# Kernel tuning notes

Measured on AMD Instinct MI355X. Metric: run time of the kernel, lower is better.

## Reference

```python
import math
import jax, jax.numpy as jnp
from jax import lax
import numpy as np

D = 256; H = 8; NL = 6; HALF = D // 2
B = 32; NEV = 256

def sinpos(x):
    # SinusoidalPosEmb: (..., ) int -> (..., D)
    freq = jnp.exp(jnp.arange(HALF, dtype=jnp.float32) * (-math.log(10000.0) / (HALF - 1)))
    e = x.astype(jnp.float32)[..., None] * freq
    return jnp.concatenate([jnp.sin(e), jnp.cos(e)], axis=-1)

def layer_norm(x, g, b, eps=1e-5):
    m = x.mean(-1, keepdims=True)
    v = ((x - m) ** 2).mean(-1, keepdims=True)
    return (x - m) / jnp.sqrt(v + eps) * g + b

def gelu(x):
    return jax.nn.gelu(x, approximate=False)

def conv1d(x, w, b, stride):
    y = lax.conv_general_dilated(x, w, (stride,), [(3, 3)], dimension_numbers=("NCH", "OIH", "NCH"))
    return y + b[None, :, None]

def setup_inputs():
    ks = iter(jax.random.split(jax.random.key(0), 48))
    def p(*shape):
        return jax.random.normal(next(ks), shape, dtype=jnp.float32) * 0.02
    inp = dict(
        mel=jax.random.normal(next(ks), (B, 80, 2000), dtype=jnp.float32),
        events=jnp.sort(jax.random.randint(next(ks), (B, NEV), 0, 2000), axis=-1),
        event_mask=jnp.zeros((B, NEV), dtype=bool),
        star_rating=jax.random.uniform(next(ks), (B,), dtype=jnp.float32) * 9.0,
        mel_W=p(16, 80), mel_b=p(16),
        conv1_w=p(128, 16, 7), conv1_b=p(128),
        gn_g=jnp.ones(128, jnp.float32), gn_b=jnp.zeros(128, jnp.float32),
        conv2_w=p(256, 128, 7), conv2_b=p(256),
        cn_g=jnp.ones(D, jnp.float32), cn_b=jnp.zeros(D, jnp.float32),
        star_table=p(20, D),
        ep_W1=p(D, 3 * D), ep_b1=p(D), ep_W2=p(D, D), ep_b2=p(D),
        tl_Wqkv=p(NL, 3 * D, D), tl_bqkv=p(NL, 3 * D),
        tl_Wo=p(NL, D, D), tl_bo=p(NL, D),
        tl_ln1g=jnp.ones((NL, D), jnp.float32), tl_ln1b=jnp.zeros((NL, D), jnp.float32),
        tl_ln2g=jnp.ones((NL, D), jnp.float32), tl_ln2b=jnp.zeros((NL, D), jnp.float32),
        tl_W1=p(NL, 4 * D, D), tl_b1=p(NL, 4 * D),
        tl_W2=p(NL, D, 4 * D), tl_b2=p(NL, D),
        pool_q=jax.random.normal(next(ks), (D,), dtype=jnp.float32),
        on_g=jnp.ones(D, jnp.float32), on_b=jnp.zeros(D, jnp.float32),
        oh_W=p(1, D), oh_b=p(1),
    )
    return inp

def reference(mel, events, event_mask, star_rating, mel_W, mel_b, conv1_w, conv1_b, gn_g, gn_b, conv2_w, conv2_b, cn_g, cn_b, star_table, ep_W1, ep_b1, ep_W2, ep_b2, tl_Wqkv, tl_bqkv, tl_Wo, tl_bo, tl_ln1g, tl_ln1b, tl_ln2g, tl_ln2b, tl_W1, tl_b1, tl_W2, tl_b2, pool_q, on_g, on_b, oh_W, oh_b):
    Bsz = mel.shape[0]
    # mel_compress on channel dim: (B,80,T) -> (B,16,T)
    x_mel = jnp.einsum('bct,oc->bot', mel, mel_W) + mel_b[None, :, None]
    h = gelu(conv1d(x_mel, conv1_w, conv1_b, 2))           # (B,128,1000)
    # GroupNorm(1, C): normalize over (C, L) per sample
    m = h.mean((1, 2), keepdims=True)
    v = ((h - m) ** 2).mean((1, 2), keepdims=True)
    h = (h - m) / jnp.sqrt(v + 1e-5) * gn_g[None, :, None] + gn_b[None, :, None]
    h = gelu(conv1d(h, conv2_w, conv2_b, 2))               # (B,256,500)
    x = h.transpose(0, 2, 1)                               # (B,500,256)
    x = layer_norm(x, cn_g, cn_b)
    S = x.shape[1]
    x = x + sinpos(jnp.arange(S))[None]
    star_bucket = jnp.clip((star_rating / 0.5).astype(jnp.int32), 0, star_table.shape[0] - 1)
    x = x + star_table[star_bucket][:, None, :]
    # --- event gap/ratio embeddings (vectorized; exact match to torch loop when all valid) ---
    diff = jnp.maximum(events[:, 1:] - events[:, :-1], 1)  # clamp(min=1)
    g = jnp.concatenate([diff[:, :1], diff], axis=1)        # g[0] = g[1]
    gap_ms = g * 5
    g_f = jnp.maximum(g.astype(jnp.float32), 1.0)
    r = jnp.clip(g_f[:, 1:] / g_f[:, :-1], 0.1, 10.0)
    ones = jnp.ones((Bsz, 1), dtype=jnp.float32)
    ratio_before = (jnp.concatenate([ones, r], axis=1) * 50).astype(jnp.int32)
    ratio_after = (jnp.concatenate([r, ones], axis=1) * 50).astype(jnp.int32)
    combined = jnp.concatenate([sinpos(ratio_before), sinpos(ratio_after), sinpos(gap_ms)], axis=-1)
    ev = gelu(combined @ ep_W1.T + ep_b1) @ ep_W2.T + ep_b2
    ev = jnp.where(event_mask[..., None], 0.0, ev)
    token_pos = jnp.clip(events // 4, 0, S - 1)
    # batched scatter-add of event embeddings into token stream
    x = x.at[jnp.arange(Bsz)[:, None], token_pos].add(ev)
    hd = D // H
    for i in range(NL):
        xn = layer_norm(x, tl_ln1g[i], tl_ln1b[i])
        qkv = xn @ tl_Wqkv[i].T + tl_bqkv[i]
        q, k, vv = jnp.split(qkv, 3, axis=-1)
        q = q.reshape(Bsz, S, H, hd).transpose(0, 2, 1, 3)
        k = k.reshape(Bsz, S, H, hd).transpose(0, 2, 1, 3)
        vv = vv.reshape(Bsz, S, H, hd).transpose(0, 2, 1, 3)
        a = jax.nn.softmax(jnp.einsum('bhqd,bhkd->bhqk', q, k) / math.sqrt(hd), axis=-1)
        o = jnp.einsum('bhqk,bhkd->bhqd', a, vv).transpose(0, 2, 1, 3).reshape(Bsz, S, D)
        x = x + o @ tl_Wo[i].T + tl_bo[i]
        xn = layer_norm(x, tl_ln2g[i], tl_ln2b[i])
        x = x + gelu(xn @ tl_W1[i].T + tl_b1[i]) @ tl_W2[i].T + tl_b2[i]
    # attention pooling + head
    logits = x @ pool_q / math.sqrt(D)
    w = jax.nn.softmax(logits, axis=-1)
    pooled = jnp.einsum('bs,bsd->bd', w, x)
    return (layer_norm(pooled, on_g, on_b) @ oh_W.T + oh_b).squeeze(-1)
```

## Files before the change

### kernel.cpp

```cpp
#include <hip/hip_runtime.h>
#include <math.h>

namespace {
constexpr int kB = 32;
constexpr int kS = 500;
constexpr int kH = 8;
}
#define LKC (-0.07252236513366287)

typedef __attribute__((ext_vector_type(8))) short s16x8;
typedef __attribute__((ext_vector_type(4))) float f32x4;

__device__ __forceinline__ float gelu_f(float x){
  return 0.5f * x * (1.0f + erff(x * 0.7071067811865476f));
}
__device__ __forceinline__ float b2f(short s){
  union { unsigned u; float f; } x; x.u = ((unsigned)(unsigned short)s) << 16; return x.f;
}
__device__ __forceinline__ short f2b(float f){
  unsigned u = __float_as_uint(f);
  unsigned r = (u + 0x7fffu + ((u >> 16) & 1u)) >> 16;
  return (short)r;
}
__device__ __forceinline__ unsigned cvtpk(float lo, float hi){
  unsigned r;
  asm("v_cvt_pk_bf16_f32 %0, %1, %2" : "=v"(r) : "v"(lo), "v"(hi));
  return r;
}

__global__ __launch_bounds__(128) void conv1w_pad(const float* __restrict__ w, short* __restrict__ out){
  int n = blockIdx.x, k = threadIdx.x;
  out[n*128 + k] = (k < 112) ? f2b(w[n*112 + k]) : (short)0;
}

__global__ __launch_bounds__(256) void f2b_all(const float* __restrict__ c2,
    const float* __restrict__ e1, const float* __restrict__ e2,
    const float* __restrict__ qk, const float* __restrict__ wo,
    const float* __restrict__ w1, const float* __restrict__ w2,
    short* __restrict__ WB){
  int blk = blockIdx.x, t = threadIdx.x;
  const float* src; short* dst; int idx;
  if(blk < 896){        src = c2; dst = WB + 16384;   idx = blk*256 + t; }
  else if(blk < 1664){  src = e1; dst = WB + 245760;  idx = (blk-896)*256 + t; }
  else if(blk < 1920){  src = e2; dst = WB + 442368;  idx = (blk-1664)*256 + t; }
  else if(blk < 6528){  src = qk; dst = WB + 507904;  idx = (blk-1920)*256 + t; }
  else if(blk < 8064){  src = wo; dst = WB + 1687552; idx = (blk-6528)*256 + t; }
  else if(blk < 14208){ src = w1; dst = WB + 2080768; idx = (blk-8064)*256 + t; }
  else {                src = w2; dst = WB + 3653632; idx = (blk-14208)*256 + t; }
  dst[idx] = f2b(src[idx]);
}

template<int OUT, bool DOGELU>
__global__ __launch_bounds__(256) void gemm_mfma(const short* __restrict__ A,
    const short* __restrict__ W, const float* __restrict__ bias,
    void* __restrict__ Cv, int M, int N, int K){
  __shared__ __align__(16) short Al[128*64];
  __shared__ __align__(16) short Wl[128*64];
  const int t = threadIdx.x;
  const int wid = t >> 6, lane = t & 63;
  const int m0 = blockIdx.y * 128, n0 = blockIdx.x * 128;
  const int wr = (wid >> 1) * 64, wc = (wid & 1) * 64;
  const int frow = lane & 15, lg = lane >> 4;
  const int rA = t >> 3;
  const int sA = (t & 7) ^ (rA & 7);
  const short* Aq = A + (size_t)(m0 + rA) * K + sA * 8;
  const short* Wq = W + (size_t)(n0 + rA) * K + sA * 8;
  f32x4 acc[4][4] = {};
  for(int k0 = 0; k0 < K; k0 += 64){
    s16x8 av[4], wv[4];
    #pragma unroll
    for(int j = 0; j < 4; ++j){
      av[j] = *(const s16x8*)(Aq + k0 + (size_t)(32*j)*K);
      wv[j] = *(const s16x8*)(Wq + k0 + (size_t)(32*j)*K);
    }
    __syncthreads();
    #pragma unroll
    for(int j = 0; j < 4; ++j){
      *(s16x8*)&Al[t*8 + j*2048] = av[j];
      *(s16x8*)&Wl[t*8 + j*2048] = wv[j];
    }
    __syncthreads();
    #pragma unroll
    for(int kh = 0; kh < 2; ++kh){
      s16x8 a[4], b[4];
      #pragma unroll
      for(int mi = 0; mi < 4; ++mi){
        int r = wr + mi*16 + frow;
        a[mi] = *(const s16x8*)&Al[r*64 + (((kh*4 + lg) ^ (r & 7)) * 8)];
      }
      #pragma unroll
      for(int ni = 0; ni < 4; ++ni){
        int r = wc + ni*16 + frow;
        b[ni] = *(const s16x8*)&Wl[r*64 + (((kh*4 + lg) ^ (r & 7)) * 8)];
      }
      #pragma unroll
      for(int mi = 0; mi < 4; ++mi)
        #pragma unroll
        for(int ni = 0; ni < 4; ++ni)
          acc[mi][ni] = __builtin_amdgcn_mfma_f32_16x16x32_bf16(a[mi], b[ni], acc[mi][ni], 0, 0, 0);
    }
  }
  #pragma unroll
  for(int mi = 0; mi < 4; ++mi){
    #pragma unroll
    for(int ni = 0; ni < 4; ++ni){
      const int col = n0 + wc + ni*16 + (lane & 15);
      const float bv = bias[col];
      #pragma unroll
      for(int r = 0; r < 4; ++r){
        const int row = m0 + wr + mi*16 + (lane >> 4)*4 + r;
        float v = acc[mi][ni][r] + bv;
        if(DOGELU) v = gelu_f(v);
        if(OUT == 0) ((float*)Cv)[(size_t)row*N + col] = v;
        else if(OUT == 1) ((float*)Cv)[(size_t)row*N + col] += v;
        else ((short*)Cv)[(size_t)row*N + col] = f2b(v);
      }
    }
  }
}

template<bool DOGELU>
__global__ __launch_bounds__(512) void gemm512(const short* __restrict__ A,
    const short* __restrict__ W, const float* __restrict__ bias,
    short* __restrict__ C, int M, int N, int K){
  __shared__ __align__(16) short Al[128*64];
  __shared__ __align__(16) short Wl[256*64];
  const int t = threadIdx.x;
  const int wid = t >> 6, lane = t & 63;
  const int m0 = blockIdx.y * 128, n0 = blockIdx.x * 256;
  const int wm = wid >> 2, wn = wid & 3;
  const int frow = lane & 15, lg = lane >> 4;
  const int rA = t >> 3;
  const int sA = (t & 7) ^ (rA & 7);
  const short* Aq = A + (size_t)(m0 + rA) * K + sA * 8;
  const short* Wq = W + (size_t)(n0 + rA) * K + sA * 8;
  f32x4 acc[4][4] = {};
  for(int k0 = 0; k0 < K; k0 += 64){
    s16x8 av[2], wv[4];
    av[0] = *(const s16x8*)(Aq + k0);
    av[1] = *(const s16x8*)(Aq + k0 + (size_t)64*K);
    #pragma unroll
    for(int j = 0; j < 4; ++j)
      wv[j] = *(const s16x8*)(Wq + k0 + (size_t)(64*j)*K);
    __syncthreads();
    *(s16x8*)&Al[t*8] = av[0];
    *(s16x8*)&Al[t*8 + 4096] = av[1];
    #pragma unroll
    for(int j = 0; j < 4; ++j)
      *(s16x8*)&Wl[t*8 + j*4096] = wv[j];
    __syncthreads();
    #pragma unroll
    for(int kh = 0; kh < 2; ++kh){
      s16x8 a[4], b[4];
      #pragma unroll
      for(int mi = 0; mi < 4; ++mi){
        int r = wm*64 + mi*16 + frow;
        a[mi] = *(const s16x8*)&Al[r*64 + (((kh*4 + lg) ^ (r & 7)) * 8)];
      }
      #pragma unroll
      for(int ni = 0; ni < 4; ++ni){
        int r = wn*64 + ni*16 + frow;
        b[ni] = *(const s16x8*)&Wl[r*64 + (((kh*4 + lg) ^ (r & 7)) * 8)];
      }
      #pragma unroll
      for(int mi = 0; mi < 4; ++mi)
        #pragma unroll
        for(int ni = 0; ni < 4; ++ni)
          acc[mi][ni] = __builtin_amdgcn_mfma_f32_16x16x32_bf16(a[mi], b[ni], acc[mi][ni], 0, 0, 0);
    }
  }
  #pragma unroll
  for(int mi = 0; mi < 4; ++mi){
    #pragma unroll
    for(int ni = 0; ni < 4; ++ni){
      const int col = n0 + wn*64 + ni*16 + (lane & 15);
      const float bv = bias[col];
      #pragma unroll
      for(int r = 0; r < 4; ++r){
        const int row = m0 + wm*64 + mi*16 + (lane >> 4)*4 + r;
        float v = acc[mi][ni][r] + bv;
        if(DOGELU) v = gelu_f(v);
        C[(size_t)row*N + col] = f2b(v);
      }
    }
  }
}

template<bool DOLN>
__global__ __launch_bounds__(512) void gemm_ln(const short* __restrict__ A,
    const short* __restrict__ W, const float* __restrict__ bias,
    float* __restrict__ X, const float* __restrict__ lg_, const float* __restrict__ lb_,
    short* __restrict__ XNB, int M, int K){
  __shared__ __align__(16) short Al[64*64];
  __shared__ __align__(16) short Wl[256*64];
  __shared__ float sbuf[64][4];
  const int t = threadIdx.x;
  const int wid = t >> 6, lane = t & 63;
  const int m0 = blockIdx.y * 64;
  const int wm = wid >> 2, wn = wid & 3;
  const int frow = lane & 15, lg = lane >> 4;
  const int lq = lane & 15;
  const int rA = t >> 3;
  const int sA = (t & 7) ^ (rA & 7);
  const short* Aq = A + (size_t)(m0 + rA) * K + sA * 8;
  const short* Wq = W + (size_t)rA * K + sA * 8;
  f32x4 acc[2][4] = {};
  for(int k0 = 0; k0 < K; k0 += 64){
    s16x8 av = *(const s16x8*)(Aq + k0);
    s16x8 wv[4];
    #pragma unroll
    for(int j = 0; j < 4; ++j)
      wv[j] = *(const s16x8*)(Wq + k0 + (size_t)(64*j)*K);
    __syncthreads();
    *(s16x8*)&Al[t*8] = av;
    #pragma unroll
    for(int j = 0; j < 4; ++j)
      *(s16x8*)&Wl[t*8 + j*4096] = wv[j];
    __syncthreads();
    #pragma unroll
    for(int kh = 0; kh < 2; ++kh){
      s16x8 a[2], b[4];
      #pragma unroll
      for(int mi = 0; mi < 2; ++mi){
        int r = wm*32 + mi*16 + frow;
        a[mi] = *(const s16x8*)&Al[r*64 + (((kh*4 + lg) ^ (r & 7)) * 8)];
      }
      #pragma unroll
      for(int ni = 0; ni < 4; ++ni){
        int r = wn*64 + ni*16 + frow;
        b[ni] = *(const s16x8*)&Wl[r*64 + (((kh*4 + lg) ^ (r & 7)) * 8)];
      }
      #pragma unroll
      for(int mi = 0; mi < 2; ++mi)
        #pragma unroll
        for(int ni = 0; ni < 4; ++ni)
          acc[mi][ni] = __builtin_amdgcn_mfma_f32_16x16x32_bf16(a[mi], b[ni], acc[mi][ni], 0, 0, 0);
    }
  }
  float v[2][4][4];
  #pragma unroll
  for(int mi = 0; mi < 2; ++mi)
    #pragma unroll
    for(int ni = 0; ni < 4; ++ni){
      const int col = wn*64 + ni*16 + lq;
      const float bv = bias[col];
      #pragma unroll
      for(int r = 0; r < 4; ++r){
        const int row = m0 + wm*32 + mi*16 + lg*4 + r;
        v[mi][ni][r] = acc[mi][ni][r] + bv + X[(size_t)row*256 + col];
      }
    }
  __syncthreads();
  float vmean[2][4], vrstd[2][4];
  if(DOLN){
    #pragma unroll
    for(int mi = 0; mi < 2; ++mi)
      #pragma unroll
      for(int r = 0; r < 4; ++r){
        float s = v[mi][0][r] + v[mi][1][r] + v[mi][2][r] + v[mi][3][r];
        s += __shfl_xor(s, 1); s += __shfl_xor(s, 2);
        s += __shfl_xor(s, 4); s += __shfl_xor(s, 8);
        if(lq == 0) sbuf[wm*32 + mi*16 + lg*4 + r][wn] = s;
      }
    __syncthreads();
    #pragma unroll
    for(int mi = 0; mi < 2; ++mi)
      #pragma unroll
      for(int r = 0; r < 4; ++r){
        int rl = wm*32 + mi*16 + lg*4 + r;
        vmean[mi][r] = (sbuf[rl][0] + sbuf[rl][1] + sbuf[rl][2] + sbuf[rl][3]) * (1.f/256.f);
      }
    __syncthreads();
    #pragma unroll
    for(int mi = 0; mi < 2; ++mi)
      #pragma unroll
      for(int r = 0; r < 4; ++r){
        float q = 0.f;
        #pragma unroll
        for(int ni = 0; ni < 4; ++ni){ float d = v[mi][ni][r] - vmean[mi][r]; q += d*d; }
        q += __shfl_xor(q, 1); q += __shfl_xor(q, 2);
        q += __shfl_xor(q, 4); q += __shfl_xor(q, 8);
        if(lq == 0) sbuf[wm*32 + mi*16 + lg*4 + r][wn] = q;
      }
    __syncthreads();
    #pragma unroll
    for(int mi = 0; mi < 2; ++mi)
      #pragma unroll
      for(int r = 0; r < 4; ++r){
        int rl = wm*32 + mi*16 + lg*4 + r;
        float Q = sbuf[rl][0] + sbuf[rl][1] + sbuf[rl][2] + sbuf[rl][3];
        vrstd[mi][r] = 1.f / sqrtf(Q * (1.f/256.f) + 1e-5f);
      }
  }
  #pragma unroll
  for(int mi = 0; mi < 2; ++mi)
    #pragma unroll
    for(int ni = 0; ni < 4; ++ni){
      const int col = wn*64 + ni*16 + lq;
      float gg = 0.f, bb = 0.f;
      if(DOLN){ gg = lg_[col]; bb = lb_[col]; }
      #pragma unroll
      for(int r = 0; r < 4; ++r){
        const int row = m0 + wm*32 + mi*16 + lg*4 + r;
        float val = v[mi][ni][r];
        X[(size_t)row*256 + col] = val;
        if(DOLN)
          XNB[(size_t)row*256 + col] = f2b((val - vmean[mi][r]) * vrstd[mi][r] * gg + bb);
      }
    }
}

__global__ __launch_bounds__(256) void mel_kernel(const float* __restrict__ mel,
    const float* __restrict__ W, const float* __restrict__ bias, float* __restrict__ xm){
  __shared__ float Ws[16][80];
  __shared__ float bs[16];
  const int t = threadIdx.x;
  for(int i = t; i < 16*80; i += 256) Ws[i/80][i%80] = W[i];
  if(t < 16) bs[t] = bias[t];
  __syncthreads();
  int blk = blockIdx.x;
  int b = blk >> 3;
  int tc = (blk & 7) * 256 + t;
  if(tc >= 2000) return;
  float acc[16];
  #pragma unroll
  for(int o = 0; o < 16; ++o) acc[o] = bs[o];
  for(int c = 0; c < 80; ++c){
    float v = mel[((size_t)b*80 + c)*2000 + tc];
    #pragma unroll
    for(int o = 0; o < 16; ++o) acc[o] += v * Ws[o][c];
  }
  #pragma unroll
  for(int o = 0; o < 16; ++o) xm[((size_t)b*16 + o)*2000 + tc] = acc[o];
}

__global__ __launch_bounds__(256) void im2col1b(const float* __restrict__ xm, short* __restrict__ A){
  size_t idx = (size_t)blockIdx.x * 256 + threadIdx.x;
  int col = idx & 127;
  size_t row = idx >> 7;
  int t1 = row % 1000, b = row / 1000;
  float v = 0.f;
  if(col < 112){
    int i = col / 7, k = col % 7;
    int src = 2*t1 + k - 3;
    if(src >= 0 && src < 2000) v = xm[((size_t)b*16 + i)*2000 + src];
  }
  A[idx] = f2b(v);
}

__global__ __launch_bounds__(256) void gn_part(const float* __restrict__ h1, double* __restrict__ part){
  int blk = blockIdx.x;
  const float* p = h1 + (size_t)blk * 16000;
  int t = threadIdx.x;
  double s = 0, q = 0;
  for(int i = t; i < 16000; i += 256){ double v = p[i]; s += v; q += v*v; }
  __shared__ double rs[256], rq[256];
  rs[t] = s; rq[t] = q; __syncthreads();
  for(int s2 = 128; s2 > 0; s2 >>= 1){
    if(t < s2){ rs[t] += rs[t+s2]; rq[t] += rq[t+s2]; }
    __syncthreads();
  }
  if(t == 0){ part[blk*2] = rs[0]; part[blk*2+1] = rq[0]; }
}
__global__ __launch_bounds__(256) void gn_final(const double* __restrict__ part, float* __restrict__ stats){
  int t = threadIdx.x;
  int b = t >> 3;
  double s = part[t*2], q = part[t*2+1];
  s += __shfl_xor(s, 1); q += __shfl_xor(q, 1);
  s += __shfl_xor(s, 2); q += __shfl_xor(q, 2);
  s += __shfl_xor(s, 4); q += __shfl_xor(q, 4);
  if((t & 7) == 0){
    double mean = s / 128000.0;
    double var  = q / 128000.0 - mean*mean;
    stats[b*2]   = (float)mean;
    stats[b*2+1] = (float)(1.0 / sqrt(var + 1e-5));
  }
}

__global__ __launch_bounds__(256) void im2col2b(const float* __restrict__ h1,
    const float* __restrict__ stats, const float* __restrict__ gg,
    const float* __restrict__ gb, short* __restrict__ A){
  size_t idx = (size_t)blockIdx.x * 256 + threadIdx.x;
  int col = idx % 896;
  size_t row = idx / 896;
  int t2 = row % 500, b = row / 500;
  int i = col / 7, k = col % 7;
  int src = 2*t2 + k - 3;
  float v = 0.f;
  if(src >= 0 && src < 1000){
    float raw = h1[((size_t)b*1000 + src)*128 + i];
    v = (raw - stats[b*2]) * stats[b*2+1] * gg[i] + gb[i];
  }
  A[idx] = f2b(v);
}

__global__ __launch_bounds__(256) void postconv(const float* __restrict__ xp,
    const float* __restrict__ cg, const float* __restrict__ cb,
    const float* __restrict__ star, const float* __restrict__ stab,
    float* __restrict__ x){
  int row = blockIdx.x, t = threadIdx.x;
  int s = row % 500, b = row / 500;
  __shared__ float red[256];
  float v = xp[(size_t)row*256 + t];
  red[t] = v; __syncthreads();
  for(int s2 = 128; s2 > 0; s2 >>= 1){ if(t < s2) red[t] += red[t+s2]; __syncthreads(); }
  float mean = red[0] / 256.f; __syncthreads();
  float d = v - mean;
  red[t] = d*d; __syncthreads();
  for(int s2 = 128; s2 > 0; s2 >>= 1){ if(t < s2) red[t] += red[t+s2]; __syncthreads(); }
  float rstd = 1.f / sqrtf(red[0]/256.f + 1e-5f);
  int j = t & 127;
  double f = exp((double)j * LKC);
  double a = (double)s * f;
  float pe = (float)(t < 128 ? sin(a) : cos(a));
  int bucket = (int)(star[b] * 2.0f);
  bucket = bucket < 0 ? 0 : (bucket > 19 ? 19 : bucket);
  x[(size_t)row*256 + t] = d*rstd*cg[t] + cb[t] + pe + stab[bucket*256 + t];
}

__global__ __launch_bounds__(256) void event_feat(const int* __restrict__ events, short* __restrict__ comb){
  int blk = blockIdx.x;
  int e = blk & 255, b = blk >> 8;
  const int* ev = events + b*256;
  int t = threadIdx.x;
  auto gof = [&](int i){ int j = i < 1 ? 1 : i; int d = ev[j] - ev[j-1]; return d < 1 ? 1 : d; };
  int gi = gof(e);
  double rb = 1.0, ra = 1.0;
  if(e != 0){
    rb = (double)gi / (double)gof(e-1);
    rb = rb < 0.1 ? 0.1 : (rb > 10.0 ? 10.0 : rb);
  }
  if(e != 255){
    ra = (double)gof(e+1) / (double)gi;
    ra = ra < 0.1 ? 0.1 : (ra > 10.0 ? 10.0 : ra);
  }
  int rbi = (int)(rb * 50.0);
  int rai = (int)(ra * 50.0);
  int gap = 5 * gi;
  int j = t & 127;
  double f = exp((double)j * LKC);
  double a0 = (double)rbi * f, a1 = (double)rai * f, a2 = (double)gap * f;
  size_t base = (size_t)blk * 768;
  comb[base + t]       = f2b((float)(t < 128 ? sin(a0) : cos(a0)));
  comb[base + 256 + t] = f2b((float)(t < 128 ? sin(a1) : cos(a1)));
  comb[base + 512 + t] = f2b((float)(t < 128 ? sin(a2) : cos(a2)));
}

__global__ __launch_bounds__(256) void ev_scatter(const float* __restrict__ evout,
    const int* __restrict__ events, const unsigned char* __restrict__ mask,
    float* __restrict__ x){
  int blk = blockIdx.x;
  int e = blk & 255, b = blk >> 8;
  if(mask[b*256 + e]) return;
  int tp = events[b*256 + e] >> 2;
  tp = tp < 0 ? 0 : (tp > 499 ? 499 : tp);
  int t = threadIdx.x;
  atomicAdd(&x[((size_t)b*500 + tp)*256 + t], evout[(size_t)blk*256 + t]);
}

__global__ __launch_bounds__(256) void ln_rows(const float* __restrict__ x,
    const float* __restrict__ g, const float* __restrict__ b, short* __restrict__ out){
  int row = blockIdx.x, t = threadIdx.x;
  int wid = t >> 6, lane = t & 63;
  __shared__ float sm[8];
  float v = x[(size_t)row*256 + t];
  float s = v;
  #pragma unroll
  for(int o = 1; o < 64; o <<= 1) s += __shfl_xor(s, o);
  if(lane == 0) sm[wid] = s;
  __syncthreads();
  float mean = (sm[0] + sm[1] + sm[2] + sm[3]) * (1.f/256.f);
  float d = v - mean;
  float q = d*d;
  #pragma unroll
  for(int o = 1; o < 64; o <<= 1) q += __shfl_xor(q, o);
  if(lane == 0) sm[4 + wid] = q;
  __syncthreads();
  float rstd = 1.f / sqrtf((sm[4] + sm[5] + sm[6] + sm[7]) * (1.f/256.f) + 1e-5f);
  out[(size_t)row*256 + t] = f2b(d*rstd*g[t] + b[t]);
}

__global__ __launch_bounds__(512) void attn_mfma(const short* __restrict__ qkv,
    short* __restrict__ o){
  __shared__ __align__(16) short Kl[256*40];
  __shared__ __align__(16) short Vt[32*264];
  __shared__ __align__(16) short Pl[8][2][640];
  const int i = blockIdx.x;
  const int b = (i & 7)*4 + ((i >> 3) & 3);
  const int qh = (i >> 5) & 1;
  const int h = (i >> 6) & 7;
  const int t = threadIdx.x;
  const int wid = t >> 6, lane = t & 63;
  const int lq = lane & 15, lg = lane >> 4;
  const short* base = qkv + (size_t)b * kS * 768;
  const float c2 = 0.17677669529663687f * 1.4426950408889634f;
  s16x8 qf[2];
  #pragma unroll
  for(int qi = 0; qi < 2; ++qi){
    int qrow = (qh*16 + wid*2 + qi)*16 + lq;
    if(qrow > kS-1) qrow = kS-1;
    qf[qi] = *(const s16x8*)(base + (size_t)qrow*768 + h*32 + lg*8);
  }
  float lsum[2] = {0.f, 0.f};
  f32x4 oa0[2] = {}, oa1[2] = {};
  for(int khalf = 0; khalf < 2; ++khalf){
    const int k0base = khalf * 256;
    if(khalf) __syncthreads();
    {
      const int c = t & 3;
      for(int idx = t; idx < 1024; idx += 512){
        int row = idx >> 2;
        int grow = k0base + row;
        s16x8 kv = {0,0,0,0,0,0,0,0};
        unsigned vu0 = 0, vu1 = 0, vu2 = 0, vu3 = 0;
        if(grow < kS){
          const short* rp = base + (size_t)grow*768 + 256 + h*32 + c*8;
          kv = *(const s16x8*)rp;
          uint4 vv = *(const uint4*)(rp + 256);
          vu0 = vv.x; vu1 = vv.y; vu2 = vv.z; vu3 = vv.w;
        }
        *(s16x8*)&Kl[row*40 + c*8] = kv;
        unsigned b0 = (c & 2) ? vu2 : vu0, b1 = (c & 2) ? vu3 : vu1;
        unsigned b2 = (c & 2) ? vu0 : vu2, b3 = (c & 2) ? vu1 : vu3;
        unsigned r0 = (c & 1) ? b1 : b0, r1 = (c & 1) ? b2 : b1;
        unsigned r2 = (c & 1) ? b3 : b2, r3 = (c & 1) ? b0 : b3;
        #pragma unroll
        for(int j0 = 0; j0 < 8; ++j0){
          unsigned w = (j0 >> 1) == 0 ? r0 : (j0 >> 1) == 1 ? r1 : (j0 >> 1) == 2 ? r2 : r3;
          short val = (short)((j0 & 1) ? (w >> 16) : (w & 0xffff));
          int d = c*8 + ((j0 + 2*c) & 7);
          Vt[d*264 + row] = val;
        }
      }
    }
    __syncthreads();
    #pragma unroll
    for(int qi = 0; qi < 2; ++qi){
      f32x4 sc[16];
      __builtin_amdgcn_s_setprio(1);
      #pragma unroll
      for(int kt = 0; kt < 16; ++kt){
        s16x8 kf = *(const s16x8*)&Kl[(kt*16 + lq)*40 + lg*8];
        f32x4 z = {0.f,0.f,0.f,0.f};
        sc[kt] = __builtin_amdgcn_mfma_f32_16x16x32_bf16(kf, qf[qi], z, 0, 0, 0);
      }
      __builtin_amdgcn_s_setprio(0);
      if(khalf == 1 && lg >= 1){ sc[15][0] = -1e30f; sc[15][1] = -1e30f; sc[15][2] = -1e30f; sc[15][3] = -1e30f; }
      float l0 = 0.f, l1 = 0.f, l2 = 0.f, l3 = 0.f;
      #pragma unroll
      for(int kt = 0; kt < 16; ++kt){
        float p0 = exp2f(sc[kt][0] * c2);
        float p1 = exp2f(sc[kt][1] * c2);
        float p2 = exp2f(sc[kt][2] * c2);
        float p3 = exp2f(sc[kt][3] * c2);
        sc[kt][0] = p0; sc[kt][1] = p1; sc[kt][2] = p2; sc[kt][3] = p3;
        l0 += p0; l1 += p1; l2 += p2; l3 += p3;
      }
      lsum[qi] += (l0 + l1) + (l2 + l3);
      #pragma unroll
      for(int kt2 = 0; kt2 < 8; ++kt2){
        short* pw = &Pl[wid][kt2 & 1][0];
        f32x4 p0 = sc[kt2*2], p1 = sc[kt2*2+1];
        uint2 pk0, pk1;
        pk0.x = cvtpk(p0[0], p0[1]); pk0.y = cvtpk(p0[2], p0[3]);
        pk1.x = cvtpk(p1[0], p1[1]); pk1.y = cvtpk(p1[2], p1[3]);
        *(uint2*)&pw[lq*40 + lg*4] = pk0;
        *(uint2*)&pw[lq*40 + 16 + lg*4] = pk1;
        s16x8 pf = *(const s16x8*)&pw[lq*40 + lg*8];
        s16x8 v0 = *(const s16x8*)&Vt[lq*264 + kt2*32 + lg*8];
        s16x8 v1 = *(const s16x8*)&Vt[(16+lq)*264 + kt2*32 + lg*8];
        __builtin_amdgcn_s_setprio(1);
        oa0[qi] = __builtin_amdgcn_mfma_f32_16x16x32_bf16(v0, pf, oa0[qi], 0, 0, 0);
        oa1[qi] = __builtin_amdgcn_mfma_f32_16x16x32_bf16(v1, pf, oa1[qi], 0, 0, 0);
        __builtin_amdgcn_s_setprio(0);
      }
    }
  }
  #pragma unroll
  for(int qi = 0; qi < 2; ++qi){
    float l = lsum[qi];
    l += __shfl_xor(l, 16, 64);
    l += __shfl_xor(l, 32, 64);
    float inv = 1.f / l;
    int qw = (qh*16 + wid*2 + qi)*16 + lq;
    if(qw < kS){
      short* op = o + ((size_t)(b*kS + qw))*256 + h*32;
      uint2 w0, w1;
      w0.x = cvtpk(oa0[qi][0]*inv, oa0[qi][1]*inv); w0.y = cvtpk(oa0[qi][2]*inv, oa0[qi][3]*inv);
      w1.x = cvtpk(oa1[qi][0]*inv, oa1[qi][1]*inv); w1.y = cvtpk(oa1[qi][2]*inv, oa1[qi][3]*inv);
      *(uint2*)&op[lg*4] = w0;
      *(uint2*)&op[16 + lg*4] = w1;
    }
  }
}

__global__ __launch_bounds__(256) void pool_head(const float* __restrict__ x,
    const float* __restrict__ pq, const float* __restrict__ og, const float* __restrict__ ob,
    const float* __restrict__ ohW, const float* __restrict__ ohb, float* __restrict__ out){
  int b = blockIdx.x, t = threadIdx.x;
  __shared__ float lg[500];
  __shared__ float red[256];
  const float* xb = x + (size_t)b * 500 * 256;
  for(int s = t; s < 500; s += 256){
    const float* xr = xb + (size_t)s * 256;
    float d = 0.f;
    for(int c = 0; c < 256; ++c) d += xr[c] * pq[c];
    lg[s] = d * 0.0625f;
  }
  __syncthreads();
  float m = -1e30f;
  for(int s = t; s < 500; s += 256) m = fmaxf(m, lg[s]);
  red[t] = m; __syncthreads();
  for(int s2 = 128; s2 > 0; s2 >>= 1){ if(t < s2) red[t] = fmaxf(red[t], red[t+s2]); __syncthreads(); }
  m = red[0]; __syncthreads();
  float ps = 0.f;
  for(int s = t; s < 500; s += 256){ float e = expf(lg[s] - m); lg[s] = e; ps += e; }
  red[t] = ps; __syncthreads();
  for(int s2 = 128; s2 > 0; s2 >>= 1){ if(t < s2) red[t] += red[t+s2]; __syncthreads(); }
  float inv = 1.f / red[0];
  __syncthreads();
  float acc = 0.f;
  for(int s = 0; s < 500; ++s) acc += lg[s] * xb[(size_t)s*256 + t];
  acc *= inv;
  __syncthreads();
  red[t] = acc; __syncthreads();
  for(int s2 = 128; s2 > 0; s2 >>= 1){ if(t < s2) red[t] += red[t+s2]; __syncthreads(); }
  float mean = red[0] / 256.f; __syncthreads();
  float d = acc - mean;
  red[t] = d*d; __syncthreads();
  for(int s2 = 128; s2 > 0; s2 >>= 1){ if(t < s2) red[t] += red[t+s2]; __syncthreads(); }
  float rstd = 1.f / sqrtf(red[0]/256.f + 1e-5f);
  __syncthreads();
  float val = (d*rstd*og[t] + ob[t]) * ohW[t];
  red[t] = val; __syncthreads();
  for(int s2 = 128; s2 > 0; s2 >>= 1){ if(t < s2) red[t] += red[t+s2]; __syncthreads(); }
  if(t == 0) out[b] = red[0] + ohb[0];
}

extern "C" void kernel_launch(void* const* d_in, const int* in_sizes, int n_in,
                              void* d_out, int out_size, void* d_ws, size_t ws_size,
                              hipStream_t stream){
  const float* mel      = (const float*)d_in[0];
  const int*   events   = (const int*)d_in[1];
  const unsigned char* emask = (const unsigned char*)d_in[2];
  const float* star     = (const float*)d_in[3];
  const float* mel_W    = (const float*)d_in[4];
  const float* mel_b    = (const float*)d_in[5];
  const float* conv1_w  = (const float*)d_in[6];
  const float* conv1_b  = (const float*)d_in[7];
  const float* gn_g     = (const float*)d_in[8];
  const float* gn_b     = (const float*)d_in[9];
  const float* conv2_w  = (const float*)d_in[10];
  const float* conv2_b  = (const float*)d_in[11];
  const float* cn_g     = (const float*)d_in[12];
  const float* cn_b     = (const float*)d_in[13];
  const float* star_tab = (const float*)d_in[14];
  const float* ep_W1    = (const float*)d_in[15];
  const float* ep_b1    = (const float*)d_in[16];
  const float* ep_W2    = (const float*)d_in[17];
  const float* ep_b2    = (const float*)d_in[18];
  const float* tl_Wqkv  = (const float*)d_in[19];
  const float* tl_bqkv  = (const float*)d_in[20];
  const float* tl_Wo    = (const float*)d_in[21];
  const float* tl_bo    = (const float*)d_in[22];
  const float* tl_ln1g  = (const float*)d_in[23];
  const float* tl_ln1b  = (const float*)d_in[24];
  const float* tl_ln2g  = (const float*)d_in[25];
  const float* tl_ln2b  = (const float*)d_in[26];
  const float* tl_W1    = (const float*)d_in[27];
  const float* tl_b1    = (const float*)d_in[28];
  const float* tl_W2    = (const float*)d_in[29];
  const float* tl_b2    = (const float*)d_in[30];
  const float* pool_q   = (const float*)d_in[31];
  const float* on_g     = (const float*)d_in[32];
  const float* on_b     = (const float*)d_in[33];
  const float* oh_W     = (const float*)d_in[34];
  const float* oh_b     = (const float*)d_in[35];
  (void)in_sizes; (void)n_in; (void)out_size; (void)ws_size;

  float* ws  = (float*)d_ws;
  float* X   = ws;
  short* XNB = (short*)(ws + 4096000);
  short* OB  = (short*)(ws + 6144000);
  short* WB  = (short*)(ws + 8192000);
  float* BIG = ws + 10812000;
  double* PART = (double*)(ws + 28668000);
  float* STATS = ws + 28671900;

  short* WBc1 = WB + 0;
  short* WBc2 = WB + 16384;
  short* WBe1 = WB + 245760;
  short* WBe2 = WB + 442368;
  short* WBqk = WB + 507904;
  short* WBwo = WB + 1687552;
  short* WBw1 = WB + 2080768;
  short* WBw2 = WB + 3653632;

  float* XMEL = BIG;
  short* A1B  = (short*)(BIG + 1024000);
  float* H1   = BIG + 3072000;
  short* A2B  = (short*)(BIG + 7168000);
  float* XPRE = BIG;
  short* COMBB= (short*)BIG;
  short* EHIDB= (short*)(BIG + 3146000);
  float* EVO  = BIG + 4195000;
  short* QKVB = (short*)BIG;
  short* HIDB = (short*)(BIG + 7168000);

  conv1w_pad<<<128, 128, 0, stream>>>(conv1_w, WBc1);
  f2b_all<<<20352, 256, 0, stream>>>(conv2_w, ep_W1, ep_W2, tl_Wqkv, tl_Wo, tl_W1, tl_W2, WB);

  mel_kernel<<<kB*8, 256, 0, stream>>>(mel, mel_W, mel_b, XMEL);
  im2col1b<<<16000, 256, 0, stream>>>(XMEL, A1B);
  gemm_mfma<0,true><<<dim3(1, 250), 256, 0, stream>>>(A1B, WBc1, conv1_b, H1, 32000, 128, 128);
  gn_part<<<256, 256, 0, stream>>>(H1, PART);
  gn_final<<<1, 256, 0, stream>>>(PART, STATS);
  im2col2b<<<56000, 256, 0, stream>>>(H1, STATS, gn_g, gn_b, A2B);
  gemm_mfma<0,true><<<dim3(2, 125), 256, 0, stream>>>(A2B, WBc2, conv2_b, XPRE, 16000, 256, 896);
  postconv<<<16000, 256, 0, stream>>>(XPRE, cn_g, cn_b, star, star_tab, X);
  event_feat<<<kB*256, 256, 0, stream>>>(events, COMBB);
  gemm_mfma<2,true><<<dim3(2, 64), 256, 0, stream>>>(COMBB, WBe1, ep_b1, EHIDB, 8192, 256, 768);
  gemm_mfma<0,false><<<dim3(2, 64), 256, 0, stream>>>(EHIDB, WBe2, ep_b2, EVO, 8192, 256, 256);
  ev_scatter<<<kB*256, 256, 0, stream>>>(EVO, events, emask, X);

  ln_rows<<<16000, 256, 0, stream>>>(X, tl_ln1g, tl_ln1b, XNB);
  for(int i = 0; i < 6; ++i){
    gemm512<false><<<dim3(3, 125), 512, 0, stream>>>(XNB, WBqk + (size_t)i*196608, tl_bqkv + i*768, QKVB, 16000, 768, 256);
    attn_mfma<<<512, 512, 0, stream>>>(QKVB, OB);
    gemm_ln<true><<<dim3(1, 250), 512, 0, stream>>>(OB, WBwo + (size_t)i*65536, tl_bo + i*256,
        X, tl_ln2g + i*256, tl_ln2b + i*256, XNB, 16000, 256);
    gemm512<true><<<dim3(4, 125), 512, 0, stream>>>(XNB, WBw1 + (size_t)i*262144, tl_b1 + i*1024, HIDB, 16000, 1024, 256);
    if(i < 5)
      gemm_ln<true><<<dim3(1, 250), 512, 0, stream>>>(HIDB, WBw2 + (size_t)i*262144, tl_b2 + i*256,
          X, tl_ln1g + (i+1)*256, tl_ln1b + (i+1)*256, XNB, 16000, 1024);
    else
      gemm_ln<false><<<dim3(1, 250), 512, 0, stream>>>(HIDB, WBw2 + (size_t)i*262144, tl_b2 + i*256,
          X, tl_ln1g, tl_ln1b, XNB, 16000, 1024);
  }

  pool_head<<<kB, 256, 0, stream>>>(X, pool_q, on_g, on_b, oh_W, oh_b, (float*)d_out);
}
```

Measured before the change: 844.4 us.

## Fuse residual-GEMM+LayerNorm with following projection GEMM in one kernel

Adds a gemm_fused kernel that computes a residual GEMM (Wo or W2), applies LayerNorm into shared memory, and immediately multiplies the normalized tile by the next layer's weights (W1 with GELU, or next QKV). This removes the XNB round trip through global memory and two kernel launches per layer. In exchange, only 250 blocks run, each doing a serial loop over 256-column output chunks, which reduces parallelism, and shared memory use per block grows.

```diff
diff --git a/kernel.cpp b/kernel.cpp
--- a/kernel.cpp
+++ b/kernel.cpp
@@ -308,6 +308,175 @@
           XNB[(size_t)row*256 + col] = f2b((val - vmean[mi][r]) * vrstd[mi][r] * gg + bb);
       }
     }
+}
+
+template<bool DOGELU2>
+__global__ __launch_bounds__(512) void gemm_fused(const short* __restrict__ A1,
+    const short* __restrict__ W1, const float* __restrict__ b1,
+    float* __restrict__ X, const float* __restrict__ lng, const float* __restrict__ lnb,
+    const short* __restrict__ W2, const float* __restrict__ b2,
+    short* __restrict__ C2, int M, int K1, int N2){
+  __shared__ __align__(16) short Al[64*64];
+  __shared__ __align__(16) short Wl[256*64];
+  __shared__ __align__(16) short XNl[64*264];
+  __shared__ float sbuf[64][4];
+  const int t = threadIdx.x;
+  const int wid = t >> 6, lane = t & 63;
+  const int m0 = blockIdx.x * 64;
+  const int wm = wid >> 2, wn = wid & 3;
+  const int frow = lane & 15, lg = lane >> 4;
+  const int lq = lane & 15;
+  const int rA = t >> 3;
+  const int sA = (t & 7) ^ (rA & 7);
+  const short* Aq = A1 + (size_t)(m0 + rA) * K1 + sA * 8;
+  const short* Wq = W1 + (size_t)rA * K1 + sA * 8;
+  f32x4 acc[2][4] = {};
+  for(int k0 = 0; k0 < K1; k0 += 64){
+    s16x8 av = *(const s16x8*)(Aq + k0);
+    s16x8 wv[4];
+    #pragma unroll
+    for(int j = 0; j < 4; ++j)
+      wv[j] = *(const s16x8*)(Wq + k0 + (size_t)(64*j)*K1);
+    __syncthreads();
+    *(s16x8*)&Al[t*8] = av;
+    #pragma unroll
+    for(int j = 0; j < 4; ++j)
+      *(s16x8*)&Wl[t*8 + j*4096] = wv[j];
+    __syncthreads();
+    #pragma unroll
+    for(int kh = 0; kh < 2; ++kh){
+      s16x8 a[2], b[4];
+      #pragma unroll
+      for(int mi = 0; mi < 2; ++mi){
+        int r = wm*32 + mi*16 + frow;
+        a[mi] = *(const s16x8*)&Al[r*64 + (((kh*4 + lg) ^ (r & 7)) * 8)];
+      }
+      #pragma unroll
+      for(int ni = 0; ni < 4; ++ni){
+        int r = wn*64 + ni*16 + frow;
+        b[ni] = *(const s16x8*)&Wl[r*64 + (((kh*4 + lg) ^ (r & 7)) * 8)];
+      }
+      #pragma unroll
+      for(int mi = 0; mi < 2; ++mi)
+        #pragma unroll
+        for(int ni = 0; ni < 4; ++ni)
+          acc[mi][ni] = __builtin_amdgcn_mfma_f32_16x16x32_bf16(a[mi], b[ni], acc[mi][ni], 0, 0, 0);
+    }
+  }
+  float v[2][4][4];
+  #pragma unroll
+  for(int mi = 0; mi < 2; ++mi)
+    #pragma unroll
+    for(int ni = 0; ni < 4; ++ni){
+      const int col = wn*64 + ni*16 + lq;
+      const float bv = b1[col];
+      #pragma unroll
+      for(int r = 0; r < 4; ++r){
+        const int row = m0 + wm*32 + mi*16 + lg*4 + r;
+        v[mi][ni][r] = acc[mi][ni][r] + bv + X[(size_t)row*256 + col];
+      }
+    }
+  __syncthreads();
+  float vmean[2][4], vrstd[2][4];
+  #pragma unroll
+  for(int mi = 0; mi < 2; ++mi)
+    #pragma unroll
+    for(int r = 0; r < 4; ++r){
+      float s = v[mi][0][r] + v[mi][1][r] + v[mi][2][r] + v[mi][3][r];
+      s += __shfl_xor(s, 1); s += __shfl_xor(s, 2);
+      s += __shfl_xor(s, 4); s += __shfl_xor(s, 8);
+      if(lq == 0) sbuf[wm*32 + mi*16 + lg*4 + r][wn] = s;
+    }
+  __syncthreads();
+  #pragma unroll
+  for(int mi = 0; mi < 2; ++mi)
+    #pragma unroll
+    for(int r = 0; r < 4; ++r){
+      int rl = wm*32 + mi*16 + lg*4 + r;
+      vmean[mi][r] = (sbuf[rl][0] + sbuf[rl][1] + sbuf[rl][2] + sbuf[rl][3]) * (1.f/256.f);
+    }
+  __syncthreads();
+  #pragma unroll
+  for(int mi = 0; mi < 2; ++mi)
+    #pragma unroll
+    for(int r = 0; r < 4; ++r){
+      float q = 0.f;
+      #pragma unroll
+      for(int ni = 0; ni < 4; ++ni){ float d = v[mi][ni][r] - vmean[mi][r]; q += d*d; }
+      q += __shfl_xor(q, 1); q += __shfl_xor(q, 2);
+      q += __shfl_xor(q, 4); q += __shfl_xor(q, 8);
+      if(lq == 0) sbuf[wm*32 + mi*16 + lg*4 + r][wn] = q;
+    }
+  __syncthreads();
+  #pragma unroll
+  for(int mi = 0; mi < 2; ++mi)
+    #pragma unroll
+    for(int r = 0; r < 4; ++r){
+      int rl = wm*32 + mi*16 + lg*4 + r;
+      float Q = sbuf[rl][0] + sbuf[rl][1] + sbuf[rl][2] + sbuf[rl][3];
+      vrstd[mi][r] = 1.f / sqrtf(Q * (1.f/256.f) + 1e-5f);
+    }
+  #pragma unroll
+  for(int mi = 0; mi < 2; ++mi)
+    #pragma unroll
+    for(int ni = 0; ni < 4; ++ni){
+      const int col = wn*64 + ni*16 + lq;
+      const float gg = lng[col], bb = lnb[col];
+      #pragma unroll
+      for(int r = 0; r < 4; ++r){
+        const int rowl = wm*32 + mi*16 + lg*4 + r;
+        float val = v[mi][ni][r];
+        X[(size_t)(m0 + rowl)*256 + col] = val;
+        XNl[rowl*264 + col] = f2b((val - vmean[mi][r]) * vrstd[mi][r] * gg + bb);
+      }
+    }
+  for(int nc = 0; nc < N2; nc += 256){
+    f32x4 acc2[2][4] = {};
+    const short* Wq2 = W2 + (size_t)(nc + rA) * 256 + sA * 8;
+    #pragma unroll
+    for(int k0 = 0; k0 < 256; k0 += 64){
+      s16x8 wv[4];
+      #pragma unroll
+      for(int j = 0; j < 4; ++j)
+        wv[j] = *(const s16x8*)(Wq2 + k0 + (size_t)(64*j)*256);
+      __syncthreads();
+      #pragma unroll
+      for(int j = 0; j < 4; ++j)
+        *(s16x8*)&Wl[t*8 + j*4096] = wv[j];
+      __syncthreads();
+      #pragma unroll
+      for(int kh = 0; kh < 2; ++kh){
+        s16x8 a[2], b[4];
+        #pragma unroll
+        for(int mi = 0; mi < 2; ++mi)
+          a[mi] = *(const s16x8*)&XNl[(wm*32 + mi*16 + frow)*264 + k0 + kh*32 + lg*8];
+        #pragma unroll
+        for(int ni = 0; ni < 4; ++ni){
+          int r = wn*64 + ni*16 + frow;
+          b[ni] = *(const s16x8*)&Wl[r*64 + (((kh*4 + lg) ^ (r & 7)) * 8)];
+        }
+        #pragma unroll
+        for(int mi = 0; mi < 2; ++mi)
+          #pragma unroll
+          for(int ni = 0; ni < 4; ++ni)
+            acc2[mi][ni] = __builtin_amdgcn_mfma_f32_16x16x32_bf16(a[mi], b[ni], acc2[mi][ni], 0, 0, 0);
+      }
+    }
+    #pragma unroll
+    for(int mi = 0; mi < 2; ++mi)
+      #pragma unroll
+      for(int ni = 0; ni < 4; ++ni){
+        const int col = nc + wn*64 + ni*16 + lq;
+        const float bv = b2[col];
+        #pragma unroll
+        for(int r = 0; r < 4; ++r){
+          const int row = m0 + wm*32 + mi*16 + lg*4 + r;
+          float vv = acc2[mi][ni][r] + bv;
+          if(DOGELU2) vv = gelu_f(vv);
+          C2[(size_t)row*N2 + col] = f2b(vv);
+        }
+      }
+  }
 }
 
 __global__ __launch_bounds__(256) void mel_kernel(const float* __restrict__ mel,
@@ -724,15 +893,16 @@
   ev_scatter<<<kB*256, 256, 0, stream>>>(EVO, events, emask, X);
 
   ln_rows<<<16000, 256, 0, stream>>>(X, tl_ln1g, tl_ln1b, XNB);
+  gemm512<false><<<dim3(3, 125), 512, 0, stream>>>(XNB, WBqk, tl_bqkv, QKVB, 16000, 768, 256);
   for(int i = 0; i < 6; ++i){
-    gemm512<false><<<dim3(3, 125), 512, 0, stream>>>(XNB, WBqk + (size_t)i*196608, tl_bqkv + i*768, QKVB, 16000, 768, 256);
     attn_mfma<<<512, 512, 0, stream>>>(QKVB, OB);
-    gemm_ln<true><<<dim3(1, 250), 512, 0, stream>>>(OB, WBwo + (size_t)i*65536, tl_bo + i*256,
-        X, tl_ln2g + i*256, tl_ln2b + i*256, XNB, 16000, 256);
-    gemm512<true><<<dim3(4, 125), 512, 0, stream>>>(XNB, WBw1 + (size_t)i*262144, tl_b1 + i*1024, HIDB, 16000, 1024, 256);
+    gemm_fused<true><<<250, 512, 0, stream>>>(OB, WBwo + (size_t)i*65536, tl_bo + i*256,
+        X, tl_ln2g + i*256, tl_ln2b + i*256,
+        WBw1 + (size_t)i*262144, tl_b1 + i*1024, HIDB, 16000, 256, 1024);
     if(i < 5)
-      gemm_ln<true><<<dim3(1, 250), 512, 0, stream>>>(HIDB, WBw2 + (size_t)i*262144, tl_b2 + i*256,
-          X, tl_ln1g + (i+1)*256, tl_ln1b + (i+1)*256, XNB, 16000, 1024);
+      gemm_fused<false><<<250, 512, 0, stream>>>(HIDB, WBw2 + (size_t)i*262144, tl_b2 + i*256,
+          X, tl_ln1g + (i+1)*256, tl_ln1b + (i+1)*256,
+          WBqk + (size_t)(i+1)*196608, tl_bqkv + (i+1)*768, QKVB, 16000, 1024, 768);
     else
       gemm_ln<false><<<dim3(1, 250), 512, 0, stream>>>(HIDB, WBw2 + (size_t)i*262144, tl_b2 + i*256,
           X, tl_ln1g, tl_ln1b, XNB, 16000, 1024);
```

After: 869.8 us. +3.0%, slower.
